# Kernel optimization log

Hardware: AMD Instinct MI355X
Metric: run time of the kernel (lower is better)

Reference implementation:

```python
import math
import jax, jax.numpy as jnp
import numpy as np

AZI = 0.006135923151542565
INC = 0.008267349088394194
EPS = 1e-6
NUM_GROUPS = 32


def group_norm(x, weight, bias, num_groups=NUM_GROUPS, eps=EPS):
    B, C, H, W = x.shape
    xg = x.reshape(B, num_groups, C // num_groups, H, W)
    mean = xg.mean(axis=(2, 3, 4), keepdims=True)
    var = xg.var(axis=(2, 3, 4), keepdims=True)
    xg = (xg - mean) * jax.lax.rsqrt(var + eps)
    x = xg.reshape(B, C, H, W)
    return x * weight[None, :, None, None] + bias[None, :, None, None]


def conv1x1(x, w, b):
    # x: [B,C,H,W], w: [O,C], b: [O]
    return jnp.einsum('bchw,oc->bohw', x, w) + b[None, :, None, None]


def edge_conv(x, r, w1, b1, w2, b2, azi=AZI, inc=INC):
    out = None
    for shift_h in (-1, 0, 1):
        for shift_w in (-1, 0, 1):
            x_s = jnp.roll(x, shift=(shift_w, shift_h), axis=(2, 3))
            r_s = jnp.roll(r, shift=(shift_w, shift_h), axis=(2, 3))
            ca, sa = math.cos(shift_w * azi), math.sin(shift_w * azi)
            ci, si = math.cos(shift_h * inc), math.sin(shift_h * inc)
            pe0 = r_s * (ca * ci) - r
            pe1 = r_s * (ca * si)
            pe2 = r_s * sa
            inp = jnp.concatenate((x_s, x, pe0, pe1, pe2), axis=1)
            h = jax.nn.relu(conv1x1(inp, w1, b1))
            h = conv1x1(h, w2, b2)
            out = h if out is None else jnp.maximum(out, h)
    return out


def setup_inputs() -> dict:
    key = jax.random.key(0)
    ks = jax.random.split(key, 12)
    B, C, W, H = 4, 64, 64, 1024
    O = 64
    Cin1 = 2 * C + 3
    Cin2 = 2 * O + 3

    def lin(k, o, i):
        return jax.random.normal(k, (o, i), dtype=jnp.float32) * (1.0 / np.sqrt(i))

    return {
        'x': jax.random.normal(ks[0], (B, C, W, H), dtype=jnp.float32),
        'r': jax.random.uniform(ks[1], (B, 1, W, H), dtype=jnp.float32),
        'n1_w': jnp.ones((C,), jnp.float32),
        'n1_b': jnp.zeros((C,), jnp.float32),
        'c1_w1': lin(ks[2], O, Cin1),
        'c1_b1': jnp.zeros((O,), jnp.float32),
        'c1_w2': lin(ks[3], O, O),
        'c1_b2': jnp.zeros((O,), jnp.float32),
        'n2_w': jnp.ones((O,), jnp.float32),
        'n2_b': jnp.zeros((O,), jnp.float32),
        'c2_w1': lin(ks[4], O, Cin2),
        'c2_b1': jnp.zeros((O,), jnp.float32),
        'c2_w2': lin(ks[5], O, O),
        'c2_b2': jnp.zeros((O,), jnp.float32),
    }


def reference(x, r, n1_w, n1_b, c1_w1, c1_b1, c1_w2, c1_b2,
              n2_w, n2_b, c2_w1, c2_b1, c2_w2, c2_b2):
    h = group_norm(x, n1_w, n1_b)
    h = jax.nn.relu(h)
    h = edge_conv(h, r, c1_w1, c1_b1, c1_w2, c1_b2)
    h = group_norm(h, n2_w, n2_b)
    h = jax.nn.relu(h)
    # dropout p=0.0 -> identity
    h = edge_conv(h, r, c2_w1, c2_b1, c2_w2, c2_b2)
    return x + h
```

## Files before the change

### kernel.cpp

```cpp
#include <hip/hip_runtime.h>
#include <hip/hip_bf16.h>
#include <cmath>
#include <math.h>

namespace {

constexpr int Bn = 4;
constexpr int Cn = 64;
constexpr int Wn = 64;
constexpr int Hn = 1024;
constexpr int HWn = Wn * Hn;
constexpr int CHWn = Cn * HWn;

typedef float f32x4 __attribute__((ext_vector_type(4)));
typedef short bf16x8 __attribute__((ext_vector_type(8)));
union Frag { uint4 u; bf16x8 s; };

constexpr float kCA[3] = {0.9999811753f, 1.0f, 0.9999811753f};
constexpr float kSA[3] = {-0.0061358846f, 0.0f, 0.0061358846f};
constexpr float kCI[3] = {0.9999658257f, 1.0f, 0.9999658257f};
constexpr float kSI[3] = {-0.0082672549f, 0.0f, 0.0082672549f};

__device__ inline unsigned packbf(float a, float b) {
  union { __hip_bfloat162 h; unsigned u; } c;
  c.h = __float22bfloat162_rn(make_float2(a, b));
  return c.u;
}
__device__ inline float bflo(unsigned d) { return __uint_as_float(d << 16); }
__device__ inline float bfhi(unsigned d) { return __uint_as_float(d & 0xFFFF0000u); }

__device__ inline void gload16(const void* g, void* l) {
  __builtin_amdgcn_global_load_lds(
      (const __attribute__((address_space(1))) void*)g,
      (__attribute__((address_space(3))) void*)l, 16, 0, 0);
}

__global__ __launch_bounds__(256) void gn_partial_kernel(
    const float* __restrict__ x, float* __restrict__ partial) {
  const int bg = blockIdx.x >> 4, part = blockIdx.x & 15;
  const float4* base = (const float4*)(x + (size_t)bg * 2 * HWn) + part * 2048;
  float s = 0.f, s2 = 0.f;
  for (int i = threadIdx.x; i < 2048; i += 256) {
    const float4 v = base[i];
    s += v.x + v.y + v.z + v.w;
    s2 += v.x * v.x + v.y * v.y + v.z * v.z + v.w * v.w;
  }
  #pragma unroll
  for (int off = 32; off > 0; off >>= 1) {
    s  += __shfl_down(s, off, 64);
    s2 += __shfl_down(s2, off, 64);
  }
  __shared__ float red[8];
  const int wid = threadIdx.x >> 6, lid = threadIdx.x & 63;
  if (lid == 0) { red[wid * 2] = s; red[wid * 2 + 1] = s2; }
  __syncthreads();
  if (threadIdx.x == 0) {
    float ts = red[0] + red[2] + red[4] + red[6];
    float t2 = red[1] + red[3] + red[5] + red[7];
    atomicAdd(&partial[bg * 2], ts);
    atomicAdd(&partial[bg * 2 + 1], t2);
  }
}

__global__ void gn_final_kernel(const float* __restrict__ partial,
                                float* __restrict__ stats) {
  const int i = threadIdx.x;
  if (i < 128) {
    const float inv = 1.0f / (2.0f * HWn);
    const float mean = partial[2 * i] * inv;
    const float var = partial[2 * i + 1] * inv - mean * mean;
    stats[2 * i] = mean;
    stats[2 * i + 1] = rsqrtf(var + 1e-6f);
  }
}

__global__ void pack_weights_kernel(const float* __restrict__ w1,
                                    const float* __restrict__ w2,
                                    ushort* __restrict__ w1a, ushort* __restrict__ w1b,
                                    ushort* __restrict__ w2p,
                                    float* __restrict__ vs9, float* __restrict__ pw0) {
  const int t = threadIdx.x;
  for (int i = t; i < 64 * 32; i += 256) {
    const int o = i >> 5, kp = (i & 31) * 2;
    *(unsigned*)&w1a[o * 64 + kp] = packbf(w1[o * 131 + kp], w1[o * 131 + kp + 1]);
    *(unsigned*)&w1b[o * 64 + kp] = packbf(w1[o * 131 + 64 + kp], w1[o * 131 + 64 + kp + 1]);
    *(unsigned*)&w2p[o * 64 + kp] = packbf(w2[o * 64 + kp], w2[o * 64 + kp + 1]);
  }
  if (t < 64) pw0[t] = w1[t * 131 + 128];
  for (int i = t; i < 9 * 64; i += 256) {
    const int s = i >> 6, k = i & 63;
    const int isw = s / 3, ish = s % 3;
    const float m0 = kCA[isw] * kCI[ish];
    const float m1 = kCA[isw] * kSI[ish];
    const float m2 = kSA[isw];
    vs9[s * 64 + k] = m0 * w1[k * 131 + 128] + m1 * w1[k * 131 + 129] +
                      m2 * w1[k * 131 + 130];
  }
}

__global__ __launch_bounds__(256, 3) void dual_gemm_kernel(
    const float* __restrict__ x, const float* __restrict__ stats,
    const float* __restrict__ gw, const float* __restrict__ gb,
    const ushort* __restrict__ w1a, const ushort* __restrict__ w1b,
    const float* __restrict__ b1,
    ushort* __restrict__ Y, ushort* __restrict__ Z) {
  __shared__ float2 scsh[64];
  __shared__ float bias[64];
  __shared__ __align__(16) ushort dsY[64 * 72];
  __shared__ __align__(16) ushort dsZ[64 * 72];
  const int blk = blockIdx.x;
  const int h0 = (blk & 15) * 64;
  const int w  = (blk >> 4) & 63;
  const int b  = blk >> 10;
  const int t  = threadIdx.x;
  const int lane = t & 63, wv = t >> 6;
  const int n = lane & 15, q = lane >> 4;

  if (t < 64) {
    const int g = t >> 1;
    const float mean = stats[(b * 32 + g) * 2];
    const float rstd = stats[(b * 32 + g) * 2 + 1];
    const float sc = rstd * gw[t];
    scsh[t] = make_float2(sc, gb[t] - mean * sc);
    bias[t] = b1[t];
  }
  __syncthreads();

  const int jg = h0 + wv * 16 + n;
  const float* xb = x + (size_t)b * CHWn + (size_t)w * Hn;
  Frag Bf[2];
  #pragma unroll
  for (int kh = 0; kh < 2; kh++) {
    unsigned d[4];
    #pragma unroll
    for (int p = 0; p < 4; p++) {
      const int c0 = kh * 32 + q * 8 + p * 2;
      const float2 s0 = scsh[c0], s1 = scsh[c0 + 1];
      const float v0 = fmaxf(xb[(size_t)c0 * HWn + jg] * s0.x + s0.y, 0.f);
      const float v1 = fmaxf(xb[(size_t)(c0 + 1) * HWn + jg] * s1.x + s1.y, 0.f);
      d[p] = packbf(v0, v1);
    }
    Bf[kh].u = make_uint4(d[0], d[1], d[2], d[3]);
  }

  f32x4 accY[4], accZ[4];
  #pragma unroll
  for (int os = 0; os < 4; os++) { accY[os] = (f32x4)0.f; accZ[os] = (f32x4)0.f; }

  #pragma unroll
  for (int os = 0; os < 4; os++) {
    const int o = os * 16 + n;
    #pragma unroll
    for (int kh = 0; kh < 2; kh++) {
      const int k = kh * 32 + q * 8;
      Frag fa, fb;
      fa.u = *(const uint4*)&w1a[o * 64 + k];
      fb.u = *(const uint4*)&w1b[o * 64 + k];
      accY[os] = __builtin_amdgcn_mfma_f32_16x16x32_bf16(fa.s, Bf[kh].s, accY[os], 0, 0, 0);
      accZ[os] = __builtin_amdgcn_mfma_f32_16x16x32_bf16(fb.s, Bf[kh].s, accZ[os], 0, 0, 0);
    }
  }

  const int jl = wv * 16 + n;
  #pragma unroll
  for (int os = 0; os < 4; os++) {
    #pragma unroll
    for (int rp = 0; rp < 4; rp += 2) {
      const int o = os * 16 + q * 4 + rp;
      *(unsigned*)&dsY[jl * 72 + o] = packbf(accY[os][rp], accY[os][rp + 1]);
      *(unsigned*)&dsZ[jl * 72 + o] =
          packbf(accZ[os][rp] + bias[o], accZ[os][rp + 1] + bias[o + 1]);
    }
  }
  __syncthreads();

  #pragma unroll
  for (int p = 0; p < 2; p++) {
    const int slot = t + 256 * p;
    const int j = slot >> 3, og = slot & 7;
    const size_t gidx = (((size_t)b * Wn + w) * Hn + h0 + j) * 64 + og * 8;
    *(uint4*)&Y[gidx] = *(const uint4*)&dsY[j * 72 + og * 8];
    *(uint4*)&Z[gidx] = *(const uint4*)&dsZ[j * 72 + og * 8];
  }
}

__global__ __launch_bounds__(256, 3) void shift_max_kernel(
    const ushort* __restrict__ Y, const ushort* __restrict__ Z,
    const float* __restrict__ r, const float* __restrict__ vs9,
    const float* __restrict__ pw0, const ushort* __restrict__ w2p,
    const float* __restrict__ b2,
    const float* __restrict__ xres, const int add_res,
    float* __restrict__ out) {
  __shared__ __align__(16) ushort ys3[3][66 * 64];
  __shared__ __align__(16) ushort w2l[64 * 64];
  __shared__ float rsh[3][68];
  __shared__ __align__(16) float vsl[9 * 64];
  const int blk = blockIdx.x;
  const int h0 = (blk & 15) * 64;
  const int w  = (blk >> 4) & 63;
  const int b  = blk >> 10;
  const int t  = threadIdx.x;
  const int lane = t & 63, wv = t >> 6;
  const int n = lane & 15, q = lane >> 4;
  const int jl = wv * 16 + n;

  const ushort* Yb = Y + (size_t)b * (size_t)Wn * Hn * 64;

  auto stage_col = [&](int wi, int wsrc) {
    const size_t ybase = (size_t)wsrc * (Hn * 64);
    #pragma unroll
    for (int p = 0; p < 3; p++) {
      const int slot = t + 256 * p;
      if (slot < 66 * 8) {
        const int jj = slot >> 3, S = slot & 7;
        const int G = S ^ (jj & 7);
        const int hsrc = (h0 + jj - 1 + 1024) & 1023;
        gload16(&Yb[ybase + (size_t)hsrc * 64 + G * 8],
                &ys3[wi][(wv * 64 + 256 * p) * 8]);
      }
    }
  };

  stage_col(0, (w + 63) & 63);
  stage_col(1, w);
  stage_col(2, (w + 1) & 63);

  #pragma unroll
  for (int i0 = 0; i0 < 2; i0++) {
    const int i = t + i0 * 256;
    const int o = i >> 3, g = i & 7;
    *(uint4*)&w2l[o * 64 + (g ^ (o & 7)) * 8] = *(const uint4*)&w2p[o * 64 + g * 8];
  }
  if (t < 144) ((float4*)vsl)[t] = ((const float4*)vs9)[t];
  for (int i = t; i < 3 * 66; i += 256) {
    const int wi = i / 66, jj = i - wi * 66;
    const int wsrc = (w + wi - 1 + 64) & 63;
    const int hsrc = (h0 + jj - 1 + 1024) & 1023;
    rsh[wi][jj] = r[(size_t)b * HWn + wsrc * Hn + hsrc];
  }

  const float rc = r[(size_t)b * HWn + (size_t)w * Hn + h0 + jl];
  float zcA[8], zcB[8];
  {
    const size_t zbase = (((size_t)b * Wn + w) * Hn + h0 + jl) * 64;
    const uint4 z0 = *(const uint4*)&Z[zbase + q * 8];
    const uint4 z1 = *(const uint4*)&Z[zbase + 32 + q * 8];
    const float4 pwA0 = *(const float4*)&pw0[q * 8];
    const float4 pwA1 = *(const float4*)&pw0[q * 8 + 4];
    const float4 pwB0 = *(const float4*)&pw0[32 + q * 8];
    const float4 pwB1 = *(const float4*)&pw0[32 + q * 8 + 4];
    const float pwA[8] = {pwA0.x, pwA0.y, pwA0.z, pwA0.w, pwA1.x, pwA1.y, pwA1.z, pwA1.w};
    const float pwB[8] = {pwB0.x, pwB0.y, pwB0.z, pwB0.w, pwB1.x, pwB1.y, pwB1.z, pwB1.w};
    const unsigned zw0[4] = {z0.x, z0.y, z0.z, z0.w};
    const unsigned zw1[4] = {z1.x, z1.y, z1.z, z1.w};
    #pragma unroll
    for (int p = 0; p < 4; p++) {
      zcA[2 * p]     = bflo(zw0[p]) - rc * pwA[2 * p];
      zcA[2 * p + 1] = bfhi(zw0[p]) - rc * pwA[2 * p + 1];
      zcB[2 * p]     = bflo(zw1[p]) - rc * pwB[2 * p];
      zcB[2 * p + 1] = bfhi(zw1[p]) - rc * pwB[2 * p + 1];
    }
  }

  __syncthreads();

  f32x4 om[4];
  #pragma unroll
  for (int os = 0; os < 4; os++) om[os] = (f32x4)(-INFINITY);

  #pragma unroll 1
  for (int sw = -1; sw <= 1; sw++) {
    const int isw = sw + 1;
    const ushort* ysb = &ys3[1 - sw][0];
    #pragma unroll
    for (int sh = -1; sh <= 1; sh++) {
      const int ish = sh + 1;
      const float rsv = rsh[1 - sw][jl - sh + 1];
      const float* vrow = &vsl[(isw * 3 + ish) * 64];
      const int ro = jl - sh + 1;
      Frag Bf0, Bf1;
      {
        const float4 vA0 = *(const float4*)&vrow[q * 8];
        const float4 vA1 = *(const float4*)&vrow[q * 8 + 4];
        const float vsA[8] = {vA0.x, vA0.y, vA0.z, vA0.w, vA1.x, vA1.y, vA1.z, vA1.w};
        const uint4 y0 = *(const uint4*)&ysb[ro * 64 + (q ^ (ro & 7)) * 8];
        const unsigned yw0[4] = {y0.x, y0.y, y0.z, y0.w};
        unsigned hw0[4];
        #pragma unroll
        for (int p = 0; p < 4; p++) {
          const float hA0 = fmaf(rsv, vsA[2 * p],     bflo(yw0[p]) + zcA[2 * p]);
          const float hA1 = fmaf(rsv, vsA[2 * p + 1], bfhi(yw0[p]) + zcA[2 * p + 1]);
          hw0[p] = packbf(fmaxf(hA0, 0.f), fmaxf(hA1, 0.f));
        }
        Bf0.u = make_uint4(hw0[0], hw0[1], hw0[2], hw0[3]);
      }
      {
        const float4 vB0 = *(const float4*)&vrow[32 + q * 8];
        const float4 vB1 = *(const float4*)&vrow[32 + q * 8 + 4];
        const float vsB[8] = {vB0.x, vB0.y, vB0.z, vB0.w, vB1.x, vB1.y, vB1.z, vB1.w};
        const uint4 y1 = *(const uint4*)&ysb[ro * 64 + ((q + 4) ^ (ro & 7)) * 8];
        const unsigned yw1[4] = {y1.x, y1.y, y1.z, y1.w};
        unsigned hw1[4];
        #pragma unroll
        for (int p = 0; p < 4; p++) {
          const float hB0 = fmaf(rsv, vsB[2 * p],     bflo(yw1[p]) + zcB[2 * p]);
          const float hB1 = fmaf(rsv, vsB[2 * p + 1], bfhi(yw1[p]) + zcB[2 * p + 1]);
          hw1[p] = packbf(fmaxf(hB0, 0.f), fmaxf(hB1, 0.f));
        }
        Bf1.u = make_uint4(hw1[0], hw1[1], hw1[2], hw1[3]);
      }
      #pragma unroll
      for (int os = 0; os < 4; os++) {
        const int orow = (os * 16 + n) * 64;
        Frag fa0, fa1;
        fa0.u = *(const uint4*)&w2l[orow + (q ^ (n & 7)) * 8];
        fa1.u = *(const uint4*)&w2l[orow + ((4 + q) ^ (n & 7)) * 8];
        f32x4 acc = (f32x4)0.f;
        acc = __builtin_amdgcn_mfma_f32_16x16x32_bf16(fa0.s, Bf0.s, acc, 0, 0, 0);
        acc = __builtin_amdgcn_mfma_f32_16x16x32_bf16(fa1.s, Bf1.s, acc, 0, 0, 0);
        #pragma unroll
        for (int e = 0; e < 4; e++) om[os][e] = fmaxf(om[os][e], acc[e]);
      }
    }
  }

  const int jgl = h0 + jl;
  #pragma unroll
  for (int os = 0; os < 4; os++) {
    #pragma unroll
    for (int e = 0; e < 4; e++) {
      const int o = os * 16 + q * 4 + e;
      const size_t idx = ((size_t)b * Cn + o) * HWn + (size_t)w * Hn + jgl;
      float v = om[os][e] + b2[o];
      if (add_res) v += xres[idx];
      out[idx] = v;
    }
  }
}

}

extern "C" void kernel_launch(void* const* d_in, const int* in_sizes, int n_in,
                              void* d_out, int out_size, void* d_ws, size_t ws_size,
                              hipStream_t stream) {
  const float* x    = (const float*)d_in[0];
  const float* r    = (const float*)d_in[1];
  const float* n1w  = (const float*)d_in[2];
  const float* n1b  = (const float*)d_in[3];
  const float* c1w1 = (const float*)d_in[4];
  const float* c1b1 = (const float*)d_in[5];
  const float* c1w2 = (const float*)d_in[6];
  const float* c1b2 = (const float*)d_in[7];
  const float* n2w  = (const float*)d_in[8];
  const float* n2b  = (const float*)d_in[9];
  const float* c2w1 = (const float*)d_in[10];
  const float* c2b1 = (const float*)d_in[11];
  const float* c2w2 = (const float*)d_in[12];
  const float* c2b2 = (const float*)d_in[13];
  float* out = (float*)d_out;

  float* partial = (float*)d_ws;
  float* statsf  = partial + 256;
  float* vs9     = partial + 512;
  float* pw0     = partial + 1088;
  ushort* Ybf = (ushort*)((char*)d_ws + 8192);
  ushort* Zbf = Ybf + (size_t)Bn * Wn * Hn * 64;
  ushort* w1a = Zbf + (size_t)Bn * Wn * Hn * 64;
  ushort* w1b = w1a + 64 * 64;
  ushort* w2p = w1b + 64 * 64;

  hipMemsetAsync(partial, 0, 256 * sizeof(float), stream);
  gn_partial_kernel<<<2048, 256, 0, stream>>>(x, partial);
  gn_final_kernel<<<1, 128, 0, stream>>>(partial, statsf);
  pack_weights_kernel<<<1, 256, 0, stream>>>(c1w1, c1w2, w1a, w1b, w2p, vs9, pw0);
  dual_gemm_kernel<<<4096, 256, 0, stream>>>(x, statsf, n1w, n1b, w1a, w1b, c1b1, Ybf, Zbf);
  shift_max_kernel<<<4096, 256, 0, stream>>>(Ybf, Zbf, r, vs9, pw0, w2p, c1b2, x, 0, out);
  hipMemsetAsync(partial, 0, 256 * sizeof(float), stream);
  gn_partial_kernel<<<2048, 256, 0, stream>>>(out, partial);
  gn_final_kernel<<<1, 128, 0, stream>>>(partial, statsf);
  pack_weights_kernel<<<1, 256, 0, stream>>>(c2w1, c2w2, w1a, w1b, w2p, vs9, pw0);
  dual_gemm_kernel<<<4096, 256, 0, stream>>>(out, statsf, n2w, n2b, w1a, w1b, c2b1, Ybf, Zbf);
  shift_max_kernel<<<4096, 256, 0, stream>>>(Ybf, Zbf, r, vs9, pw0, w2p, c2b2, x, 1, out);
}
```

Baseline: 354.7 us.

## Fuse second group-norm statistics into shift_max epilogue and merge prep kernels

Accumulates per-group sum and sum-of-squares inside the first shift_max kernel's output epilogue, using shared-memory atomics followed by global atomics. This removes the separate gn_partial pass that re-read the full intermediate output. It also merges gn_final and pack_weights into one prep kernel to cut launches, and raises the launch_bounds occupancy hint from 3 to 4. The shared-memory atomics add contention in the epilogue, and the tighter register budget could cause spills.

New measurement: 463.4 us. +30.7%, slower.

```diff
diff --git a/kernel.cpp b/kernel.cpp
--- a/kernel.cpp
+++ b/kernel.cpp
@@ -62,24 +62,21 @@
   }
 }
 
-__global__ void gn_final_kernel(const float* __restrict__ partial,
-                                float* __restrict__ stats) {
-  const int i = threadIdx.x;
-  if (i < 128) {
+__global__ void prep_kernel(const float* __restrict__ partial,
+                            float* __restrict__ stats,
+                            const float* __restrict__ w1,
+                            const float* __restrict__ w2,
+                            ushort* __restrict__ w1a, ushort* __restrict__ w1b,
+                            ushort* __restrict__ w2p,
+                            float* __restrict__ vs9, float* __restrict__ pw0) {
+  const int t = threadIdx.x;
+  if (t < 128) {
     const float inv = 1.0f / (2.0f * HWn);
-    const float mean = partial[2 * i] * inv;
-    const float var = partial[2 * i + 1] * inv - mean * mean;
-    stats[2 * i] = mean;
-    stats[2 * i + 1] = rsqrtf(var + 1e-6f);
-  }
-}
-
-__global__ void pack_weights_kernel(const float* __restrict__ w1,
-                                    const float* __restrict__ w2,
-                                    ushort* __restrict__ w1a, ushort* __restrict__ w1b,
-                                    ushort* __restrict__ w2p,
-                                    float* __restrict__ vs9, float* __restrict__ pw0) {
-  const int t = threadIdx.x;
+    const float mean = partial[2 * t] * inv;
+    const float var = partial[2 * t + 1] * inv - mean * mean;
+    stats[2 * t] = mean;
+    stats[2 * t + 1] = rsqrtf(var + 1e-6f);
+  }
   for (int i = t; i < 64 * 32; i += 256) {
     const int o = i >> 5, kp = (i & 31) * 2;
     *(unsigned*)&w1a[o * 64 + kp] = packbf(w1[o * 131 + kp], w1[o * 131 + kp + 1]);
@@ -184,17 +181,19 @@
   }
 }
 
-__global__ __launch_bounds__(256, 3) void shift_max_kernel(
+__global__ __launch_bounds__(256, 4) void shift_max_kernel(
     const ushort* __restrict__ Y, const ushort* __restrict__ Z,
     const float* __restrict__ r, const float* __restrict__ vs9,
     const float* __restrict__ pw0, const ushort* __restrict__ w2p,
     const float* __restrict__ b2,
     const float* __restrict__ xres, const int add_res,
-    float* __restrict__ out) {
+    float* __restrict__ out,
+    float* __restrict__ partial, const int do_stats) {
   __shared__ __align__(16) ushort ys3[3][66 * 64];
   __shared__ __align__(16) ushort w2l[64 * 64];
   __shared__ float rsh[3][68];
   __shared__ __align__(16) float vsl[9 * 64];
+  __shared__ float gsum[32], gsum2[32];
   const int blk = blockIdx.x;
   const int h0 = (blk & 15) * 64;
   const int w  = (blk >> 4) & 63;
@@ -225,6 +224,7 @@
   stage_col(1, w);
   stage_col(2, (w + 1) & 63);
 
+  if (t < 32) { gsum[t] = 0.f; gsum2[t] = 0.f; }
   #pragma unroll
   for (int i0 = 0; i0 < 2; i0++) {
     const int i = t + i0 * 256;
@@ -328,12 +328,26 @@
   #pragma unroll
   for (int os = 0; os < 4; os++) {
     #pragma unroll
-    for (int e = 0; e < 4; e++) {
-      const int o = os * 16 + q * 4 + e;
-      const size_t idx = ((size_t)b * Cn + o) * HWn + (size_t)w * Hn + jgl;
-      float v = om[os][e] + b2[o];
-      if (add_res) v += xres[idx];
-      out[idx] = v;
+    for (int pr = 0; pr < 2; pr++) {
+      const int o0 = os * 16 + q * 4 + pr * 2;
+      const size_t idx0 = ((size_t)b * Cn + o0) * HWn + (size_t)w * Hn + jgl;
+      float v0 = om[os][pr * 2] + b2[o0];
+      float v1 = om[os][pr * 2 + 1] + b2[o0 + 1];
+      if (add_res) { v0 += xres[idx0]; v1 += xres[idx0 + HWn]; }
+      out[idx0] = v0;
+      out[idx0 + HWn] = v1;
+      if (do_stats) {
+        const int g = os * 8 + q * 2 + pr;
+        atomicAdd(&gsum[g], v0 + v1);
+        atomicAdd(&gsum2[g], v0 * v0 + v1 * v1);
+      }
+    }
+  }
+  if (do_stats) {
+    __syncthreads();
+    if (t < 32) {
+      atomicAdd(&partial[(b * 32 + t) * 2], gsum[t]);
+      atomicAdd(&partial[(b * 32 + t) * 2 + 1], gsum2[t]);
     }
   }
 }
@@ -371,14 +385,13 @@
 
   hipMemsetAsync(partial, 0, 256 * sizeof(float), stream);
   gn_partial_kernel<<<2048, 256, 0, stream>>>(x, partial);
-  gn_final_kernel<<<1, 128, 0, stream>>>(partial, statsf);
-  pack_weights_kernel<<<1, 256, 0, stream>>>(c1w1, c1w2, w1a, w1b, w2p, vs9, pw0);
+  prep_kernel<<<1, 256, 0, stream>>>(partial, statsf, c1w1, c1w2, w1a, w1b, w2p, vs9, pw0);
   dual_gemm_kernel<<<4096, 256, 0, stream>>>(x, statsf, n1w, n1b, w1a, w1b, c1b1, Ybf, Zbf);
-  shift_max_kernel<<<4096, 256, 0, stream>>>(Ybf, Zbf, r, vs9, pw0, w2p, c1b2, x, 0, out);
   hipMemsetAsync(partial, 0, 256 * sizeof(float), stream);
-  gn_partial_kernel<<<2048, 256, 0, stream>>>(out, partial);
-  gn_final_kernel<<<1, 128, 0, stream>>>(partial, statsf);
-  pack_weights_kernel<<<1, 256, 0, stream>>>(c2w1, c2w2, w1a, w1b, w2p, vs9, pw0);
+  shift_max_kernel<<<4096, 256, 0, stream>>>(Ybf, Zbf, r, vs9, pw0, w2p, c1b2,
+                                             x, 0, out, partial, 1);
+  prep_kernel<<<1, 256, 0, stream>>>(partial, statsf, c2w1, c2w2, w1a, w1b, w2p, vs9, pw0);
   dual_gemm_kernel<<<4096, 256, 0, stream>>>(out, statsf, n2w, n2b, w1a, w1b, c2b1, Ybf, Zbf);
-  shift_max_kernel<<<4096, 256, 0, stream>>>(Ybf, Zbf, r, vs9, pw0, w2p, c2b2, x, 1, out);
-}
+  shift_max_kernel<<<4096, 256, 0, stream>>>(Ybf, Zbf, r, vs9, pw0, w2p, c2b2,
+                                             x, 1, out, partial, 0);
+}
```
